# Optimization experiments

Measured on AMD Instinct MI355X. Metric: run time of the kernel, lower is better.

The kernel has to match this reference:

```python
import jax, jax.numpy as jnp
import numpy as np

UNITS = 512
EPS = 1e-6

def setup_inputs() -> dict:
    key = jax.random.key(0)
    x = jax.random.normal(key, (262144, UNITS), dtype=jnp.float32)
    return {"x": x}

def reference(x):
    d = x.shape[1]
    # Gram matrix with diagonal jitter: [d, d]
    g = x.T @ x + jnp.eye(d, dtype=x.dtype) * EPS
    L = jnp.linalg.cholesky(g)  # lower triangular [d, d]
    # inv(L) via triangular solve (same math as tf.linalg.inv on L)
    L_inv = jax.scipy.linalg.solve_triangular(L, jnp.eye(d, dtype=x.dtype), lower=True)
    ortho_weights = L_inv.T * jnp.sqrt(jnp.float32(UNITS))
    return x @ ortho_weights
```

## Files before the change

kernel.cpp:

```cpp
#include <hip/hip_runtime.h>


#define EPSJ 1e-6f
#define SQRTD 22.627416997969522f

typedef short bf16x8 __attribute__((ext_vector_type(8)));
typedef float f32x4 __attribute__((ext_vector_type(4)));

__device__ __forceinline__ unsigned short f2bf(float f) {
  unsigned u = __float_as_uint(f);
  unsigned r = u + 0x7fffu + ((u >> 16) & 1u);
  return (unsigned short)(r >> 16);
}

__device__ __forceinline__ int swz(int row, int slot) {
  return slot ^ ((row ^ (row >> 3)) & 7);
}

__device__ __forceinline__ float wred(float s) {
  s += __shfl_xor(s, 1);  s += __shfl_xor(s, 2);  s += __shfl_xor(s, 4);
  s += __shfl_xor(s, 8);  s += __shfl_xor(s, 16); s += __shfl_xor(s, 32);
  return s;
}

#define GLOAD16(g, l)                                                         \
  __builtin_amdgcn_global_load_lds(                                           \
      (const __attribute__((address_space(1))) void*)(g),                     \
      (__attribute__((address_space(3))) void*)(l), 16, 0, 0)

__global__ void convert_bf(const float* __restrict__ X,
                           unsigned short* __restrict__ Xbf) {
  long idx = (long)blockIdx.x * blockDim.x + threadIdx.x;
  const long stride = (long)gridDim.x * blockDim.x;
  const long nch = 134217728 / 8;
  for (long i = idx; i < nch; i += stride) {
    float4 f0 = ((const float4*)X)[i * 2];
    float4 f1 = ((const float4*)X)[i * 2 + 1];
    uint4 o;
    o.x = (unsigned)f2bf(f0.x) | ((unsigned)f2bf(f0.y) << 16);
    o.y = (unsigned)f2bf(f0.z) | ((unsigned)f2bf(f0.w) << 16);
    o.z = (unsigned)f2bf(f1.x) | ((unsigned)f2bf(f1.y) << 16);
    o.w = (unsigned)f2bf(f1.z) | ((unsigned)f2bf(f1.w) << 16);
    ((uint4*)Xbf)[i] = o;
  }
}

__device__ __forceinline__ void stage_pack(const unsigned short* __restrict__ src,
                                           unsigned short* dst, int c0, int k) {
  uint4 a = *(const uint4*)src;
  uint4 b = *(const uint4*)(src + 512);
  unsigned av[4] = {a.x, a.y, a.z, a.w}, bv[4] = {b.x, b.y, b.z, b.w};
  int k7 = (k & 7) * 2, khi = k >> 3;
  #pragma unroll
  for (int j = 0; j < 4; ++j) {
    int cA = c0 + 2 * j, cB = cA + 1;
    unsigned lo = (av[j] & 0xFFFFu) | (bv[j] << 16);
    unsigned hi = (av[j] >> 16) | (bv[j] & 0xFFFF0000u);
    int slA = khi ^ ((cA ^ (cA >> 3)) & 7);
    int slB = khi ^ ((cB ^ (cB >> 3)) & 7);
    *(unsigned*)((char*)dst + cA * 128 + slA * 16 + k7) = lo;
    *(unsigned*)((char*)dst + cB * 128 + slB * 16 + k7) = hi;
  }
}

__global__ __launch_bounds__(512, 2) void gram_bf(
    const unsigned short* __restrict__ Xbf, float* __restrict__ part,
    int nchunk) {
  __shared__ unsigned short As[256 * 64];
  __shared__ unsigned short Bs[256 * 64];
  const int b = blockIdx.x, pos = b % 3, chunk = b / 3;
  const int s0 = (int)((long)4096 * chunk / nchunk);
  const int s1 = (int)((long)4096 * (chunk + 1) / nchunk);
  const int ca = (pos == 1) ? 256 : 0;
  const int cb2 = (pos == 0) ? 0 : 256;
  const bool diag = (pos != 2);
  const int t = threadIdx.x, lane = t & 63, w = t >> 6;
  const int wr = w >> 2, wc = w & 3;

  f32x4 acc[8][4];
  const f32x4 zf = {0.f, 0.f, 0.f, 0.f};
  #pragma unroll
  for (int a = 0; a < 8; ++a)
    #pragma unroll
    for (int bb = 0; bb < 4; ++bb) acc[a][bb] = zf;

  const int c0 = (t & 31) * 8;
  const int kp = t >> 5;

  for (int ks = s0; ks < s1; ++ks) {
    long rb = (long)ks * 64;
    #pragma unroll
    for (int it = 0; it < 2; ++it) {
      int k = it * 32 + kp * 2;
      long r = rb + k;
      stage_pack(Xbf + r * 512 + ca + c0, As, c0, k);
      if (!diag) stage_pack(Xbf + r * 512 + cb2 + c0, Bs, c0, k);
    }
    __syncthreads();
    const unsigned short* Bp = diag ? As : Bs;
    #pragma unroll
    for (int kk = 0; kk < 2; ++kk) {
      bf16x8 af[8], bfr[4];
      #pragma unroll
      for (int fm = 0; fm < 8; ++fm) {
        int row = wr * 128 + fm * 16 + (lane & 15);
        int slot = swz(row, kk * 4 + (lane >> 4));
        af[fm] = *(const bf16x8*)((const char*)As + row * 128 + slot * 16);
      }
      #pragma unroll
      for (int fn = 0; fn < 4; ++fn) {
        int row = wc * 64 + fn * 16 + (lane & 15);
        int slot = swz(row, kk * 4 + (lane >> 4));
        bfr[fn] = *(const bf16x8*)((const char*)Bp + row * 128 + slot * 16);
      }
      #pragma unroll
      for (int fm = 0; fm < 8; ++fm)
        #pragma unroll
        for (int fn = 0; fn < 4; ++fn)
          acc[fm][fn] = __builtin_amdgcn_mfma_f32_16x16x32_bf16(
              bfr[fn], af[fm], acc[fm][fn], 0, 0, 0);
    }
    __syncthreads();
  }
  float* out = part + (long)b * 65536;
  #pragma unroll
  for (int fm = 0; fm < 8; ++fm)
    #pragma unroll
    for (int fn = 0; fn < 4; ++fn) {
      int mi = wr * 128 + fm * 16 + (lane & 15);
      int nj = wc * 64 + fn * 16 + (lane >> 4) * 4;
      *(float4*)(out + mi * 256 + nj) = *(float4*)&acc[fm][fn];
    }
}

__global__ __launch_bounds__(512, 2) void gram_f32(
    const float* __restrict__ X, float* __restrict__ part, int nchunk) {
  __shared__ unsigned short As[256 * 64];
  __shared__ unsigned short Bs[256 * 64];
  const int b = blockIdx.x;
  const int pos = b % 3;
  const int chunk = b / 3;
  const int CR = 262144 / nchunk;
  const long r0 = (long)chunk * CR;
  const int ca = (pos == 1) ? 256 : 0;
  const int cb = (pos == 0) ? 0 : 256;
  const bool diag = (pos != 2);
  const int t = threadIdx.x, lane = t & 63, w = t >> 6;
  const int wr = w >> 2, wc = w & 3;

  f32x4 acc[8][4];
  const f32x4 zf = {0.f, 0.f, 0.f, 0.f};
  #pragma unroll
  for (int a = 0; a < 8; ++a)
    #pragma unroll
    for (int bb = 0; bb < 4; ++bb) acc[a][bb] = zf;

  const int c_oct = t & 31, msub = t >> 5;

  for (int ks = 0; ks < CR; ks += 64) {
    #pragma unroll
    for (int it = 0; it < 4; ++it) {
      int m = msub + 16 * it;
      long row = r0 + ks + m;
      const float4* sa = (const float4*)(X + row * 512 + ca + c_oct * 8);
      float4 a0 = sa[0], a1 = sa[1];
      {
        float v[8] = {a0.x, a0.y, a0.z, a0.w, a1.x, a1.y, a1.z, a1.w};
        #pragma unroll
        for (int s = 0; s < 8; ++s) {
          int c = c_oct * 8 + s;
          int off = c * 128 + ((2 * m) ^ (((c ^ (c >> 3)) & 7) << 4));
          *(unsigned short*)((char*)As + off) = f2bf(v[s]);
        }
      }
      if (!diag) {
        const float4* sb = (const float4*)(X + row * 512 + cb + c_oct * 8);
        float4 b0 = sb[0], b1 = sb[1];
        float v[8] = {b0.x, b0.y, b0.z, b0.w, b1.x, b1.y, b1.z, b1.w};
        #pragma unroll
        for (int s = 0; s < 8; ++s) {
          int c = c_oct * 8 + s;
          int off = c * 128 + ((2 * m) ^ (((c ^ (c >> 3)) & 7) << 4));
          *(unsigned short*)((char*)Bs + off) = f2bf(v[s]);
        }
      }
    }
    __syncthreads();
    const unsigned short* Bp = diag ? As : Bs;
    #pragma unroll
    for (int kk = 0; kk < 2; ++kk) {
      bf16x8 af[8], bfr[4];
      #pragma unroll
      for (int fm = 0; fm < 8; ++fm) {
        int row = wr * 128 + fm * 16 + (lane & 15);
        int slot = swz(row, kk * 4 + (lane >> 4));
        af[fm] = *(const bf16x8*)((const char*)As + row * 128 + slot * 16);
      }
      #pragma unroll
      for (int fn = 0; fn < 4; ++fn) {
        int row = wc * 64 + fn * 16 + (lane & 15);
        int slot = swz(row, kk * 4 + (lane >> 4));
        bfr[fn] = *(const bf16x8*)((const char*)Bp + row * 128 + slot * 16);
      }
      #pragma unroll
      for (int fm = 0; fm < 8; ++fm)
        #pragma unroll
        for (int fn = 0; fn < 4; ++fn)
          acc[fm][fn] = __builtin_amdgcn_mfma_f32_16x16x32_bf16(
              af[fm], bfr[fn], acc[fm][fn], 0, 0, 0);
    }
    __syncthreads();
  }
  float* out = part + (long)b * 65536;
  #pragma unroll
  for (int fm = 0; fm < 8; ++fm)
    #pragma unroll
    for (int fn = 0; fn < 4; ++fn)
      #pragma unroll
      for (int j = 0; j < 4; ++j) {
        int i  = wr * 128 + fm * 16 + (lane >> 4) * 4 + j;
        int jj = wc * 64 + fn * 16 + (lane & 15);
        out[i * 256 + jj] = acc[fm][fn][j];
      }
}

__global__ void gram_reduce(const float* __restrict__ part,
                            float* __restrict__ G, int nchunk) {
  int idx = blockIdx.x * 256 + threadIdx.x;
  int pos = idx >> 16;
  int e = idx & 65535;
  float s = 0.f;
  for (int ch = 0; ch < nchunk; ++ch)
    s += part[(long)(ch * 3 + pos) * 65536 + e];
  int i = e >> 8, j = e & 255;
  if (pos == 0) {
    G[i * 512 + j] = s;
  } else if (pos == 1) {
    G[(256 + i) * 512 + 256 + j] = s;
  } else {
    G[i * 512 + 256 + j] = s;
    G[(256 + j) * 512 + i] = s;
  }
}

__global__ __launch_bounds__(256) void chol_d64(float* __restrict__ G,
                                                float* __restrict__ Dinv,
                                                int p) {
  __shared__ float Pb[64][65];
  __shared__ float Sb[64][65];
  __shared__ float Inv[64][65];
  __shared__ float Tt[32][33];
  const int t = threadIdx.x;
  const int r0 = 64 * p;
  const int tr = (t >> 4) * 4, tc = (t & 15) * 4;

  for (int idx = t; idx < 4096; idx += 256) {
    int i = idx >> 6, j = idx & 63;
    float v = G[(long)(r0 + i) * 512 + r0 + j];
    if (i == j) v += EPSJ;
    Pb[i][j] = v;
  }
  __syncthreads();

  if (p > 0) {
    float cc[4][4] = {{0.f}};
    for (int r = 0; r < p; ++r) {
      for (int idx = t; idx < 4096; idx += 256) {
        int i = idx >> 6, j = idx & 63;
        Sb[i][j] = G[(long)(r0 + i) * 512 + 64 * r + j];
      }
      __syncthreads();
      #pragma unroll 4
      for (int k = 0; k < 64; ++k) {
        float a0 = Sb[tr][k], a1 = Sb[tr+1][k], a2 = Sb[tr+2][k], a3 = Sb[tr+3][k];
        float b0 = Sb[tc][k], b1 = Sb[tc+1][k], b2 = Sb[tc+2][k], b3 = Sb[tc+3][k];
        cc[0][0]+=a0*b0; cc[0][1]+=a0*b1; cc[0][2]+=a0*b2; cc[0][3]+=a0*b3;
        cc[1][0]+=a1*b0; cc[1][1]+=a1*b1; cc[1][2]+=a1*b2; cc[1][3]+=a1*b3;
        cc[2][0]+=a2*b0; cc[2][1]+=a2*b1; cc[2][2]+=a2*b2; cc[2][3]+=a2*b3;
        cc[3][0]+=a3*b0; cc[3][1]+=a3*b1; cc[3][2]+=a3*b2; cc[3][3]+=a3*b3;
      }
      __syncthreads();
    }
    #pragma unroll
    for (int u = 0; u < 4; ++u)
      #pragma unroll
      for (int v = 0; v < 4; ++v)
        Pb[tr + u][tc + v] -= cc[u][v];
    __syncthreads();
  }

  const int lane = t & 63, w = t >> 6;
  #pragma unroll
  for (int sp = 0; sp < 2; ++sp) {
    const int b0 = sp * 32;
    if (w == 0) {
      float rr[32];
      #pragma unroll
      for (int k = 0; k < 32; ++k)
        rr[k] = (lane < 32) ? Pb[b0 + lane][b0 + k] : 0.f;
      #pragma unroll
      for (int j = 0; j < 32; ++j) {
        float d = sqrtf(__shfl(rr[j], j));
        if (lane == j) rr[j] = d;
        else if (lane > j && lane < 32) rr[j] = rr[j] / d;
        float rj = rr[j];
        #pragma unroll
        for (int k = j + 1; k < 32; ++k) {
          float Lkj = __shfl(rj, k);
          if (lane > j && lane < 32) rr[k] -= rj * Lkj;
        }
      }
      #pragma unroll
      for (int k = 0; k < 32; ++k)
        if (lane < 32) Pb[b0 + lane][b0 + k] = rr[k];
    }
    __syncthreads();
    if (sp == 0) {
      if (t < 32) {
        int rw = 32 + t;
        float x[32];
        #pragma unroll
        for (int j = 0; j < 32; ++j) x[j] = Pb[rw][j];
        #pragma unroll
        for (int j = 0; j < 32; ++j) {
          float xj = x[j] / Pb[j][j];
          x[j] = xj;
          #pragma unroll
          for (int k2 = j + 1; k2 < 32; ++k2) x[k2] -= xj * Pb[k2][j];
        }
        #pragma unroll
        for (int j = 0; j < 32; ++j) Pb[rw][j] = x[j];
      }
      __syncthreads();
      {
        int i = 32 + (t >> 3), kb = 32 + (t & 7) * 4;
        float sv[4];
        #pragma unroll
        for (int e = 0; e < 4; ++e) sv[e] = Pb[i][kb + e];
        #pragma unroll 4
        for (int j = 0; j < 32; ++j) {
          float aij = Pb[i][j];
          #pragma unroll
          for (int e = 0; e < 4; ++e) sv[e] -= aij * Pb[kb + e][j];
        }
        #pragma unroll
        for (int e = 0; e < 4; ++e) Pb[i][kb + e] = sv[e];
      }
      __syncthreads();
    }
  }

  if (t < 64) {
    int col = t & 31, o = (t >> 5) * 32;
    float x[32];
    #pragma unroll
    for (int i = 0; i < 32; ++i) {
      float s = (i == col) ? 1.f : 0.f;
      #pragma unroll
      for (int j = 0; j < i; ++j) s -= Pb[o + i][o + j] * x[j];
      x[i] = s / Pb[o + i][o + i];
    }
    #pragma unroll
    for (int i = 0; i < 32; ++i) Inv[o + i][o + col] = x[i];
  }
  for (int idx = t; idx < 1024; idx += 256)
    Inv[idx >> 5][32 + (idx & 31)] = 0.f;
  __syncthreads();
  {
    int i = t >> 3, jb = (t & 7) * 4;
    float sv[4] = {0.f, 0.f, 0.f, 0.f};
    #pragma unroll 4
    for (int k = 0; k < 32; ++k) {
      float bik = Pb[32 + i][k];
      #pragma unroll
      for (int e = 0; e < 4; ++e) sv[e] += bik * Inv[k][jb + e];
    }
    #pragma unroll
    for (int e = 0; e < 4; ++e) Tt[i][jb + e] = sv[e];
  }
  __syncthreads();
  {
    int i = t >> 3, jb = (t & 7) * 4;
    float sv[4] = {0.f, 0.f, 0.f, 0.f};
    #pragma unroll 4
    for (int k = 0; k < 32; ++k) {
      float cik = Inv[32 + i][32 + k];
      #pragma unroll
      for (int e = 0; e < 4; ++e) sv[e] += cik * Tt[k][jb + e];
    }
    #pragma unroll
    for (int e = 0; e < 4; ++e) Inv[32 + i][jb + e] = -sv[e];
  }
  __syncthreads();
  for (int idx = t; idx < 4096; idx += 256) {
    int i = idx >> 6, j = idx & 63;
    G[(long)(r0 + i) * 512 + r0 + j] = Pb[i][j];
    Dinv[p * 4096 + idx] = Inv[i][j];
  }
}

__global__ __launch_bounds__(256) void chol_t64(float* __restrict__ G,
                                                const float* __restrict__ Dinv,
                                                int p) {
  __shared__ float SbI[64][65];
  __shared__ float SbP[64][65];
  __shared__ float Ub[64][65];
  __shared__ float Db[64][65];
  const int t = threadIdx.x;
  const long rI = 64 * (p + 1 + blockIdx.x), cP = 64 * p;
  const int tr = (t >> 4) * 4, tc = (t & 15) * 4;

  for (int idx = t; idx < 4096; idx += 256)
    Db[idx >> 6][idx & 63] = Dinv[p * 4096 + idx];

  float cc[4][4] = {{0.f}};
  for (int r = 0; r < p; ++r) {
    __syncthreads();
    for (int idx = t; idx < 4096; idx += 256) {
      int i = idx >> 6, j = idx & 63;
      SbI[i][j] = G[(rI + i) * 512 + 64 * r + j];
      SbP[i][j] = G[(cP + i) * 512 + 64 * r + j];
    }
    __syncthreads();
    #pragma unroll 4
    for (int k = 0; k < 64; ++k) {
      float a0 = SbI[tr][k], a1 = SbI[tr+1][k], a2 = SbI[tr+2][k], a3 = SbI[tr+3][k];
      float b0 = SbP[tc][k], b1 = SbP[tc+1][k], b2 = SbP[tc+2][k], b3 = SbP[tc+3][k];
      cc[0][0]+=a0*b0; cc[0][1]+=a0*b1; cc[0][2]+=a0*b2; cc[0][3]+=a0*b3;
      cc[1][0]+=a1*b0; cc[1][1]+=a1*b1; cc[1][2]+=a1*b2; cc[1][3]+=a1*b3;
      cc[2][0]+=a2*b0; cc[2][1]+=a2*b1; cc[2][2]+=a2*b2; cc[2][3]+=a2*b3;
      cc[3][0]+=a3*b0; cc[3][1]+=a3*b1; cc[3][2]+=a3*b2; cc[3][3]+=a3*b3;
    }
  }
  __syncthreads();
  #pragma unroll
  for (int u = 0; u < 4; ++u)
    #pragma unroll
    for (int v = 0; v < 4; ++v)
      Ub[tr + u][tc + v] =
          G[(rI + tr + u) * 512 + cP + tc + v] - cc[u][v];
  __syncthreads();
  float xx[4][4] = {{0.f}};
  #pragma unroll 4
  for (int k = 0; k < 64; ++k) {
    float a0 = Ub[tr][k], a1 = Ub[tr+1][k], a2 = Ub[tr+2][k], a3 = Ub[tr+3][k];
    float b0 = Db[tc][k], b1 = Db[tc+1][k], b2 = Db[tc+2][k], b3 = Db[tc+3][k];
    xx[0][0]+=a0*b0; xx[0][1]+=a0*b1; xx[0][2]+=a0*b2; xx[0][3]+=a0*b3;
    xx[1][0]+=a1*b0; xx[1][1]+=a1*b1; xx[1][2]+=a1*b2; xx[1][3]+=a1*b3;
    xx[2][0]+=a2*b0; xx[2][1]+=a2*b1; xx[2][2]+=a2*b2; xx[2][3]+=a2*b3;
    xx[3][0]+=a3*b0; xx[3][1]+=a3*b1; xx[3][2]+=a3*b2; xx[3][3]+=a3*b3;
  }
  #pragma unroll
  for (int u = 0; u < 4; ++u)
    #pragma unroll
    for (int v = 0; v < 4; ++v)
      G[(rI + tr + u) * 512 + cP + tc + v] = xx[u][v];
}

__global__ __launch_bounds__(256) void tri_assemble(
    const float* __restrict__ G, const float* __restrict__ Dinv,
    unsigned short* __restrict__ Wt) {
  __shared__ float Bsh[448 * 64];
  __shared__ float T[64 * 64];
  const int q = blockIdx.x, t = threadIdx.x;
  const int or_ = (t >> 4) * 4, oc = (t & 15) * 4;

  for (int p = q + 1; p < 8; ++p) {
    float cc[4][4] = {{0.f}};
    for (int r = q; r < p; ++r) {
      const float* Lbase = G + (long)(64 * p) * 512 + 64 * r;
      #pragma unroll 4
      for (int k = 0; k < 64; ++k) {
        float a0 = Lbase[(or_ + 0) * 512 + k];
        float a1 = Lbase[(or_ + 1) * 512 + k];
        float a2 = Lbase[(or_ + 2) * 512 + k];
        float a3 = Lbase[(or_ + 3) * 512 + k];
        float b0, b1, b2, b3;
        if (r == q) {
          const float* Bq = Dinv + q * 4096 + k * 64 + oc;
          b0 = Bq[0]; b1 = Bq[1]; b2 = Bq[2]; b3 = Bq[3];
        } else {
          const float* Br = Bsh + ((r - q - 1) * 64 + k) * 64 + oc;
          b0 = Br[0]; b1 = Br[1]; b2 = Br[2]; b3 = Br[3];
        }
        cc[0][0] += a0*b0; cc[0][1] += a0*b1; cc[0][2] += a0*b2; cc[0][3] += a0*b3;
        cc[1][0] += a1*b0; cc[1][1] += a1*b1; cc[1][2] += a1*b2; cc[1][3] += a1*b3;
        cc[2][0] += a2*b0; cc[2][1] += a2*b1; cc[2][2] += a2*b2; cc[2][3] += a2*b3;
        cc[3][0] += a3*b0; cc[3][1] += a3*b1; cc[3][2] += a3*b2; cc[3][3] += a3*b3;
      }
    }
    #pragma unroll
    for (int u = 0; u < 4; ++u)
      #pragma unroll
      for (int v = 0; v < 4; ++v)
        T[(or_ + u) * 64 + oc + v] = cc[u][v];
    __syncthreads();

    float c2[4][4] = {{0.f}};
    const float* Dp = Dinv + p * 4096;
    #pragma unroll 4
    for (int k = 0; k < 64; ++k) {
      float a0 = Dp[(or_ + 0) * 64 + k];
      float a1 = Dp[(or_ + 1) * 64 + k];
      float a2 = Dp[(or_ + 2) * 64 + k];
      float a3 = Dp[(or_ + 3) * 64 + k];
      const float* Tk = T + k * 64 + oc;
      float b0 = Tk[0], b1 = Tk[1], b2 = Tk[2], b3 = Tk[3];
      c2[0][0] += a0*b0; c2[0][1] += a0*b1; c2[0][2] += a0*b2; c2[0][3] += a0*b3;
      c2[1][0] += a1*b0; c2[1][1] += a1*b1; c2[1][2] += a1*b2; c2[1][3] += a1*b3;
      c2[2][0] += a2*b0; c2[2][1] += a2*b1; c2[2][2] += a2*b2; c2[2][3] += a2*b3;
      c2[3][0] += a3*b0; c2[3][1] += a3*b1; c2[3][2] += a3*b2; c2[3][3] += a3*b3;
    }
    #pragma unroll
    for (int u = 0; u < 4; ++u)
      #pragma unroll
      for (int v = 0; v < 4; ++v)
        Bsh[((p - q - 1) * 64 + or_ + u) * 64 + oc + v] = -c2[u][v];
    __syncthreads();
  }

  const int nr = (8 - q) * 64;
  for (int idx = t; idx < nr * 64; idx += 256) {
    int i = idx >> 6, kk = idx & 63;
    float v = (i < 64) ? Dinv[q * 4096 + i * 64 + kk]
                       : Bsh[(i - 64) * 64 + kk];
    int n = 64 * q + i;
    int sl = (kk >> 3) ^ ((n ^ (n >> 3)) & 7);
    Wt[(long)n * 512 + 64 * q + sl * 8 + (kk & 7)] = f2bf(SQRTD * v);
  }
  for (int idx = t; idx < 64 * q * 64; idx += 256) {
    int n = idx >> 6, kk = idx & 63;
    Wt[(long)n * 512 + 64 * q + kk] = 0;
  }
}

__global__ void tri_inv(const float* __restrict__ G,
                        unsigned short* __restrict__ Wt) {
  int w = threadIdx.x >> 6, lane = threadIdx.x & 63;
  int c = blockIdx.x * 4 + w;
  float v8[8];
  #pragma unroll
  for (int q = 0; q < 8; ++q) v8[q] = 0.f;
  #pragma unroll
  for (int q = 0; q < 8; ++q) {
    for (int ii = 0; ii < 64; ++ii) {
      int i = q * 64 + ii;
      const float* Lrow = G + (long)i * 512;
      float s = 0.f;
      #pragma unroll
      for (int qq = 0; qq < 8; ++qq) {
        if (qq < q) s += v8[qq] * Lrow[qq * 64 + lane];
      }
      s += (lane < ii) ? v8[q] * Lrow[q * 64 + lane] : 0.f;
      s = wred(s);
      float xi = (((i == c) ? 1.f : 0.f) - s) / Lrow[i];
      if (lane == ii) v8[q] = xi;
    }
  }
  #pragma unroll
  for (int q = 0; q < 8; ++q) {
    int i = q * 64 + lane;
    Wt[(long)i * 512 + c] = f2bf(SQRTD * v8[q]);
  }
}

__global__ __launch_bounds__(256, 2) void ymm2(
    const unsigned short* __restrict__ Xbf,
    const unsigned short* __restrict__ Wt, float* __restrict__ Y) {
  __shared__ unsigned short As[2][128 * 64];
  __shared__ unsigned short Bs[2][128 * 64];
  const int t = threadIdx.x, lane = t & 63, w = t >> 6;
  const long m0 = (long)blockIdx.y * 128;
  const int n0 = blockIdx.x * 128;
  const int wm = (w >> 1) * 64, wn = (w & 1) * 64;
  const int lrow = lane >> 3, lslot = lane & 7;
  f32x4 acc[4][4];
  const f32x4 zf = {0.f, 0.f, 0.f, 0.f};
  #pragma unroll
  for (int a = 0; a < 4; ++a)
    #pragma unroll
    for (int bq = 0; bq < 4; ++bq) acc[a][bq] = zf;

  auto stage = [&](int buf, int k0) {
    #pragma unroll
    for (int j = 0; j < 4; ++j) {
      int row = (w * 4 + j) * 8 + lrow;
      const unsigned short* sA =
          Xbf + (m0 + row) * 512 + k0 + swz(row, lslot) * 8;
      const unsigned short* sB =
          Wt + (long)(n0 + row) * 512 + k0 + lslot * 8;
      GLOAD16(sA, &As[buf][(w * 4 + j) * 512]);
      GLOAD16(sB, &Bs[buf][(w * 4 + j) * 512]);
    }
  };
  auto compute = [&](int buf) {
    #pragma unroll
    for (int kk = 0; kk < 2; ++kk) {
      bf16x8 af[4], bfr[4];
      #pragma unroll
      for (int fm = 0; fm < 4; ++fm) {
        int row = wm + fm * 16 + (lane & 15);
        af[fm] = *(const bf16x8*)((const char*)As[buf] + row * 128 +
                                  swz(row, kk * 4 + (lane >> 4)) * 16);
      }
      #pragma unroll
      for (int fn = 0; fn < 4; ++fn) {
        int row = wn + fn * 16 + (lane & 15);
        bfr[fn] = *(const bf16x8*)((const char*)Bs[buf] + row * 128 +
                                   swz(row, kk * 4 + (lane >> 4)) * 16);
      }
      #pragma unroll
      for (int fm = 0; fm < 4; ++fm)
        #pragma unroll
        for (int fn = 0; fn < 4; ++fn)
          acc[fm][fn] = __builtin_amdgcn_mfma_f32_16x16x32_bf16(
              bfr[fn], af[fm], acc[fm][fn], 0, 0, 0);
    }
  };

  stage(0, 0);
  __syncthreads();
  int cur = 0;
  #pragma unroll 1
  for (int kt = 0; kt < 7; ++kt) {
    stage(cur ^ 1, (kt + 1) * 64);
    compute(cur);
    __syncthreads();
    cur ^= 1;
  }
  compute(cur);

  #pragma unroll
  for (int fm = 0; fm < 4; ++fm)
    #pragma unroll
    for (int fn = 0; fn < 4; ++fn) {
      long row = m0 + wm + fm * 16 + (lane & 15);
      int col = n0 + wn + fn * 16 + (lane >> 4) * 4;
      *(float4*)(Y + row * 512 + col) = *(float4*)&acc[fm][fn];
    }
}

__global__ __launch_bounds__(256) void ymm_v1(const float* __restrict__ X,
                                              const unsigned short* __restrict__ Wt,
                                              float* __restrict__ Y) {
  __shared__ unsigned short As[128 * 64];
  __shared__ unsigned short Bs[128 * 64];
  const int t = threadIdx.x, lane = t & 63, w = t >> 6;
  const long m0 = (long)blockIdx.x * 128;
  const int n0 = blockIdx.y * 128;
  const int wm = (w >> 1) * 64, wn = (w & 1) * 64;
  f32x4 acc[4][4];
  const f32x4 zf = {0.f, 0.f, 0.f, 0.f};
  #pragma unroll
  for (int a = 0; a < 4; ++a)
    #pragma unroll
    for (int bq = 0; bq < 4; ++bq) acc[a][bq] = zf;
  const int ko = t & 7, mrow = t >> 3;

  for (int k0 = 0; k0 < 512; k0 += 64) {
    #pragma unroll
    for (int it = 0; it < 4; ++it) {
      int m = mrow + 32 * it;
      const float4* src = (const float4*)(X + (m0 + m) * 512 + k0 + ko * 8);
      float4 f0 = src[0], f1 = src[1];
      unsigned p0 = (unsigned)f2bf(f0.x) | ((unsigned)f2bf(f0.y) << 16);
      unsigned p1 = (unsigned)f2bf(f0.z) | ((unsigned)f2bf(f0.w) << 16);
      unsigned p2 = (unsigned)f2bf(f1.x) | ((unsigned)f2bf(f1.y) << 16);
      unsigned p3 = (unsigned)f2bf(f1.z) | ((unsigned)f2bf(f1.w) << 16);
      int slot = swz(m, ko);
      *(uint4*)((char*)As + m * 128 + slot * 16) = make_uint4(p0, p1, p2, p3);
    }
    #pragma unroll
    for (int it = 0; it < 4; ++it) {
      int n = mrow + 32 * it;
      uint4 raw = *(const uint4*)(Wt + (long)(n0 + n) * 512 + k0 + ko * 8);
      int slot = swz(n, ko);
      *(uint4*)((char*)Bs + n * 128 + slot * 16) = raw;
    }
    __syncthreads();
    #pragma unroll
    for (int kk = 0; kk < 2; ++kk) {
      bf16x8 af[4], bfr[4];
      #pragma unroll
      for (int fm = 0; fm < 4; ++fm) {
        int row = wm + fm * 16 + (lane & 15);
        af[fm] = *(const bf16x8*)((const char*)As + row * 128 +
                                  swz(row, kk * 4 + (lane >> 4)) * 16);
      }
      #pragma unroll
      for (int fn = 0; fn < 4; ++fn) {
        int row = wn + fn * 16 + (lane & 15);
        bfr[fn] = *(const bf16x8*)((const char*)Bs + row * 128 +
                                   swz(row, kk * 4 + (lane >> 4)) * 16);
      }
      #pragma unroll
      for (int fm = 0; fm < 4; ++fm)
        #pragma unroll
        for (int fn = 0; fn < 4; ++fn)
          acc[fm][fn] = __builtin_amdgcn_mfma_f32_16x16x32_bf16(
              af[fm], bfr[fn], acc[fm][fn], 0, 0, 0);
    }
    __syncthreads();
  }
  #pragma unroll
  for (int fm = 0; fm < 4; ++fm)
    #pragma unroll
    for (int fn = 0; fn < 4; ++fn)
      #pragma unroll
      for (int j = 0; j < 4; ++j) {
        long row = m0 + wm + fm * 16 + (lane >> 4) * 4 + j;
        int col = n0 + wn + fn * 16 + (lane & 15);
        Y[row * 512 + col] = acc[fm][fn][j];
      }
}

static void chol_chain(float* G, float* Dinv, hipStream_t stream) {
  for (int p = 0; p < 8; ++p) {
    chol_d64<<<1, 256, 0, stream>>>(G, Dinv, p);
    if (p < 7) chol_t64<<<7 - p, 256, 0, stream>>>(G, Dinv, p);
  }
}

extern "C" void kernel_launch(void* const* d_in, const int* in_sizes, int n_in,
                              void* d_out, int out_size, void* d_ws, size_t ws_size,
                              hipStream_t stream) {
  const float* X = (const float*)d_in[0];
  float* Y = (float*)d_out;
  char* ws = (char*)d_ws;
  float* G = (float*)ws;
  unsigned short* Wt = (unsigned short*)(ws + (1 << 20));
  float* Dinv = (float*)(ws + (1 << 20) + (1 << 19));

  const int NCH_FAST = 85;
  size_t part_off = (size_t)(2 << 20);
  size_t part_bytes = (size_t)NCH_FAST * 3 * 65536 * 4;
  size_t xbf_off = part_off + part_bytes;
  size_t need = xbf_off + (size_t)134217728 * 2;

  if (ws_size >= need) {
    float* part = (float*)(ws + part_off);
    unsigned short* Xbf = (unsigned short*)(ws + xbf_off);
    convert_bf<<<2048, 256, 0, stream>>>(X, Xbf);
    gram_bf<<<3 * NCH_FAST, 512, 0, stream>>>(Xbf, part, NCH_FAST);
    gram_reduce<<<768, 256, 0, stream>>>(part, G, NCH_FAST);
    chol_chain(G, Dinv, stream);
    tri_assemble<<<8, 256, 0, stream>>>(G, Dinv, Wt);
    ymm2<<<dim3(4, 2048), 256, 0, stream>>>(Xbf, Wt, Y);
  } else {
    float* part = (float*)(ws + part_off);
    size_t fixed = part_off;
    int nchunk = 64;
    while (nchunk > 1 && fixed + (size_t)nchunk * 3 * 65536 * 4 > ws_size)
      nchunk >>= 1;
    gram_f32<<<3 * nchunk, 512, 0, stream>>>(X, part, nchunk);
    gram_reduce<<<768, 256, 0, stream>>>(part, G, nchunk);
    chol_chain(G, Dinv, stream);
    tri_inv<<<128, 256, 0, stream>>>(G, Wt);
    ymm_v1<<<dim3(2048, 4), 256, 0, stream>>>(X, Wt, Y);
  }
}
```

Baseline: 1.472 ms.

## Read weight fragments directly from global in output GEMM; remap blocks per XCD

```diff
diff --git a/kernel.cpp b/kernel.cpp
--- a/kernel.cpp
+++ b/kernel.cpp
@@ -45,21 +45,29 @@
   }
 }
 
-__device__ __forceinline__ void stage_pack(const unsigned short* __restrict__ src,
-                                           unsigned short* dst, int c0, int k) {
-  uint4 a = *(const uint4*)src;
-  uint4 b = *(const uint4*)(src + 512);
-  unsigned av[4] = {a.x, a.y, a.z, a.w}, bv[4] = {b.x, b.y, b.z, b.w};
-  int k7 = (k & 7) * 2, khi = k >> 3;
-  #pragma unroll
-  for (int j = 0; j < 4; ++j) {
-    int cA = c0 + 2 * j, cB = cA + 1;
-    unsigned lo = (av[j] & 0xFFFFu) | (bv[j] << 16);
-    unsigned hi = (av[j] >> 16) | (bv[j] & 0xFFFF0000u);
-    int slA = khi ^ ((cA ^ (cA >> 3)) & 7);
-    int slB = khi ^ ((cB ^ (cB >> 3)) & 7);
-    *(unsigned*)((char*)dst + cA * 128 + slA * 16 + k7) = lo;
-    *(unsigned*)((char*)dst + cB * 128 + slB * 16 + k7) = hi;
+__device__ __forceinline__ void stage_pack4(
+    const unsigned short* __restrict__ src,
+    unsigned short* dst, int c0, int kg) {
+  uint4 r0 = *(const uint4*)src;
+  uint4 r1 = *(const uint4*)(src + 512);
+  uint4 r2 = *(const uint4*)(src + 1024);
+  uint4 r3 = *(const uint4*)(src + 1536);
+  unsigned a[4] = {r0.x, r0.y, r0.z, r0.w};
+  unsigned b[4] = {r1.x, r1.y, r1.z, r1.w};
+  unsigned c[4] = {r2.x, r2.y, r2.z, r2.w};
+  unsigned d[4] = {r3.x, r3.y, r3.z, r3.w};
+  const int khi = kg >> 1, koff = (kg & 1) * 8;
+  #pragma unroll
+  for (int s = 0; s < 8; ++s) {
+    int wsel = s >> 1, sh = (s & 1) * 16;
+    unsigned v0 = (a[wsel] >> sh) & 0xFFFFu;
+    unsigned v1 = (b[wsel] >> sh) & 0xFFFFu;
+    unsigned v2 = (c[wsel] >> sh) & 0xFFFFu;
+    unsigned v3 = (d[wsel] >> sh) & 0xFFFFu;
+    int cc = c0 + s;
+    int sl = khi ^ ((cc ^ (cc >> 3)) & 7);
+    *(uint2*)((char*)dst + cc * 128 + sl * 16 + koff) =
+        make_uint2(v0 | (v1 << 16), v2 | (v3 << 16));
   }
 }
 
@@ -85,17 +93,12 @@
     for (int bb = 0; bb < 4; ++bb) acc[a][bb] = zf;
 
   const int c0 = (t & 31) * 8;
-  const int kp = t >> 5;
+  const int kg = t >> 5;
 
   for (int ks = s0; ks < s1; ++ks) {
-    long rb = (long)ks * 64;
-    #pragma unroll
-    for (int it = 0; it < 2; ++it) {
-      int k = it * 32 + kp * 2;
-      long r = rb + k;
-      stage_pack(Xbf + r * 512 + ca + c0, As, c0, k);
-      if (!diag) stage_pack(Xbf + r * 512 + cb2 + c0, Bs, c0, k);
-    }
+    long r = (long)ks * 64 + kg * 4;
+    stage_pack4(Xbf + r * 512 + ca + c0, As, c0, kg);
+    if (!diag) stage_pack4(Xbf + r * 512 + cb2 + c0, Bs, c0, kg);
     __syncthreads();
     const unsigned short* Bp = diag ? As : Bs;
     #pragma unroll
@@ -525,8 +528,7 @@
     float v = (i < 64) ? Dinv[q * 4096 + i * 64 + kk]
                        : Bsh[(i - 64) * 64 + kk];
     int n = 64 * q + i;
-    int sl = (kk >> 3) ^ ((n ^ (n >> 3)) & 7);
-    Wt[(long)n * 512 + 64 * q + sl * 8 + (kk & 7)] = f2bf(SQRTD * v);
+    Wt[(long)n * 512 + 64 * q + kk] = f2bf(SQRTD * v);
   }
   for (int idx = t; idx < 64 * q * 64; idx += 256) {
     int n = idx >> 6, kk = idx & 63;
@@ -564,14 +566,15 @@
   }
 }
 
-__global__ __launch_bounds__(256, 2) void ymm2(
+__global__ __launch_bounds__(256, 3) void ymm3(
     const unsigned short* __restrict__ Xbf,
     const unsigned short* __restrict__ Wt, float* __restrict__ Y) {
   __shared__ unsigned short As[2][128 * 64];
-  __shared__ unsigned short Bs[2][128 * 64];
   const int t = threadIdx.x, lane = t & 63, w = t >> 6;
-  const long m0 = (long)blockIdx.y * 128;
-  const int n0 = blockIdx.x * 128;
+  const int id = blockIdx.x;
+  const int xcd = id & 7, j = id >> 3;
+  const long m0 = (long)((j >> 2) * 8 + xcd) * 128;
+  const int n0 = (j & 3) * 128;
   const int wm = (w >> 1) * 64, wn = (w & 1) * 64;
   const int lrow = lane >> 3, lslot = lane & 7;
   f32x4 acc[4][4];
@@ -583,38 +586,11 @@
 
   auto stage = [&](int buf, int k0) {
     #pragma unroll
-    for (int j = 0; j < 4; ++j) {
-      int row = (w * 4 + j) * 8 + lrow;
+    for (int jj = 0; jj < 4; ++jj) {
+      int row = (w * 4 + jj) * 8 + lrow;
       const unsigned short* sA =
           Xbf + (m0 + row) * 512 + k0 + swz(row, lslot) * 8;
-      const unsigned short* sB =
-          Wt + (long)(n0 + row) * 512 + k0 + lslot * 8;
-      GLOAD16(sA, &As[buf][(w * 4 + j) * 512]);
-      GLOAD16(sB, &Bs[buf][(w * 4 + j) * 512]);
-    }
-  };
-  auto compute = [&](int buf) {
-    #pragma unroll
-    for (int kk = 0; kk < 2; ++kk) {
-      bf16x8 af[4], bfr[4];
-      #pragma unroll
-      for (int fm = 0; fm < 4; ++fm) {
-        int row = wm + fm * 16 + (lane & 15);
-        af[fm] = *(const bf16x8*)((const char*)As[buf] + row * 128 +
-                                  swz(row, kk * 4 + (lane >> 4)) * 16);
-      }
-      #pragma unroll
-      for (int fn = 0; fn < 4; ++fn) {
-        int row = wn + fn * 16 + (lane & 15);
-        bfr[fn] = *(const bf16x8*)((const char*)Bs[buf] + row * 128 +
-                                   swz(row, kk * 4 + (lane >> 4)) * 16);
-      }
-      #pragma unroll
-      for (int fm = 0; fm < 4; ++fm)
-        #pragma unroll
-        for (int fn = 0; fn < 4; ++fn)
-          acc[fm][fn] = __builtin_amdgcn_mfma_f32_16x16x32_bf16(
-              bfr[fn], af[fm], acc[fm][fn], 0, 0, 0);
+      GLOAD16(sA, &As[buf][(w * 4 + jj) * 512]);
     }
   };
 
@@ -622,13 +598,37 @@
   __syncthreads();
   int cur = 0;
   #pragma unroll 1
-  for (int kt = 0; kt < 7; ++kt) {
-    stage(cur ^ 1, (kt + 1) * 64);
-    compute(cur);
+  for (int kt = 0; kt < 8; ++kt) {
+    if (kt < 7) stage(cur ^ 1, (kt + 1) * 64);
+    const int k0 = kt * 64;
+    bf16x8 bfr[2][4];
+    #pragma unroll
+    for (int kk = 0; kk < 2; ++kk)
+      #pragma unroll
+      for (int fn = 0; fn < 4; ++fn) {
+        int n = n0 + wn + fn * 16 + (lane & 15);
+        bfr[kk][fn] = *(const bf16x8*)(Wt + (long)n * 512 + k0 + kk * 32 +
+                                       (lane >> 4) * 8);
+      }
+    #pragma unroll
+    for (int kk = 0; kk < 2; ++kk) {
+      bf16x8 af[4];
+      #pragma unroll
+      for (int fm = 0; fm < 4; ++fm) {
+        int row = wm + fm * 16 + (lane & 15);
+        af[fm] = *(const bf16x8*)((const char*)As[cur] + row * 128 +
+                                  swz(row, kk * 4 + (lane >> 4)) * 16);
+      }
+      #pragma unroll
+      for (int fm = 0; fm < 4; ++fm)
+        #pragma unroll
+        for (int fn = 0; fn < 4; ++fn)
+          acc[fm][fn] = __builtin_amdgcn_mfma_f32_16x16x32_bf16(
+              bfr[kk][fn], af[fm], acc[fm][fn], 0, 0, 0);
+    }
     __syncthreads();
     cur ^= 1;
   }
-  compute(cur);
 
   #pragma unroll
   for (int fm = 0; fm < 4; ++fm)
@@ -745,7 +745,7 @@
     gram_reduce<<<768, 256, 0, stream>>>(part, G, NCH_FAST);
     chol_chain(G, Dinv, stream);
     tri_assemble<<<8, 256, 0, stream>>>(G, Dinv, Wt);
-    ymm2<<<dim3(4, 2048), 256, 0, stream>>>(Xbf, Wt, Y);
+    ymm3<<<8192, 256, 0, stream>>>(Xbf, Wt, Y);
   } else {
     float* part = (float*)(ws + part_off);
     size_t fixed = part_off;
```

Result: no change. 1.500 ms (+1.9%).
